# Kernel optimization log

Hardware: AMD Instinct MI355X
Metric: run time of the kernel (lower is better)

The kernel has to match this reference:

```python
import jax, jax.numpy as jnp
import numpy as np

B_, L_, DM, E, H, R, K = 8, 2048, 512, 64, 64, 4, 3

def setup_inputs() -> dict:
    key = jax.random.key(0)
    ks = jax.random.split(key, 9)
    s = 0.02
    x = jax.random.normal(ks[0], (B_, L_, DM), dtype=jnp.float32)
    W_in = jax.random.normal(ks[1], (DM, 2 * E), dtype=jnp.float32) * s
    conv_w = jax.random.normal(ks[2], (E, K), dtype=jnp.float32) * s   # depthwise kernel per channel
    conv_b = jnp.zeros((E,), dtype=jnp.float32)
    W_x = jax.random.normal(ks[3], (E, R + 2 * H), dtype=jnp.float32) * s
    W_dt = jax.random.normal(ks[4], (R, E), dtype=jnp.float32) * s
    b_dt = jax.random.normal(ks[5], (E,), dtype=jnp.float32) * s
    A_log = jnp.log(jnp.broadcast_to(jnp.arange(1, H + 1, dtype=jnp.float32), (E, H)))
    D = jnp.ones((E,), dtype=jnp.float32)
    W_out = jax.random.normal(ks[6], (E, DM), dtype=jnp.float32) * s
    return {"x": x, "W_in": W_in, "conv_w": conv_w, "conv_b": conv_b,
            "W_x": W_x, "W_dt": W_dt, "b_dt": b_dt, "A_log": A_log, "D": D, "W_out": W_out}

def _causal_dwconv(x, w, b):
    # x: [b, l, E]; w: [E, K]; equivalent to Conv1d(groups=E, padding=K-1)[..., :l]
    xp = jnp.pad(x, ((0, 0), (K - 1, 0), (0, 0)))
    y = b
    for j in range(K):
        y = y + xp[:, j:j + x.shape[1], :] * w[:, j]
    return y

def _mamba(x, W_in, conv_w, conv_b, W_x, W_dt, b_dt, A_log, D, W_out):
    l = x.shape[1]
    xz = x @ W_in                                   # [b, l, 2E]
    xp, res = xz[..., :E], xz[..., E:]
    xp = jax.nn.silu(_causal_dwconv(xp, conv_w, conv_b))
    x_dbl = xp @ W_x                                # [b, l, R+2H]
    dlt, Bm, Cm = x_dbl[..., :R], x_dbl[..., R:R + H], x_dbl[..., R + H:]
    delta = jax.nn.softplus(dlt @ W_dt + b_dt)      # [b, l, E]
    A = -jnp.exp(A_log)                             # [E, H]
    deltaA = jnp.exp(jnp.einsum('bld,dn->bldn', delta, A))
    dBu = jnp.einsum('bld,bln,bld->bldn', delta, Bm, xp)
    state0 = jnp.zeros((x.shape[0], E, H), dtype=x.dtype)
    def step(s, inp):
        dA_t, dBu_t, C_t = inp
        s = dA_t * s + dBu_t                        # [b, E, H]
        y_t = jnp.einsum('bdn,bn->bd', s, C_t)
        return s, y_t
    xs = (jnp.swapaxes(deltaA, 0, 1), jnp.swapaxes(dBu, 0, 1), jnp.swapaxes(Cm, 0, 1))
    _, ys = jax.lax.scan(step, state0, xs)          # [l, b, E]
    y = jnp.swapaxes(ys, 0, 1) + xp * D
    y = y * jax.nn.sigmoid(res)
    return y @ W_out

def reference(x, W_in, conv_w, conv_b, W_x, W_dt, b_dt, A_log, D, W_out):
    return _mamba(x, W_in, conv_w, conv_b, W_x, W_dt, b_dt, A_log, D, W_out)
```

## Files before the change

kernel.cpp:

```cpp
#include <hip/hip_runtime.h>
#include <hip/hip_bf16.h>

#define B_ 8
#define L_ 2048
#define DM 512
#define E_ 64
#define H_ 64
#define R_ 4
#define KC 3
#define BL (B_*L_)
#define NX 132
#define LC 128
#define NCH (L_/LC)

typedef __attribute__((ext_vector_type(8))) short bfrag;
typedef __attribute__((ext_vector_type(4))) float facc;
typedef unsigned int u32;

#define LOG2E 1.4426950408889634f

__device__ __forceinline__ unsigned short f2b(float f) {
  __hip_bfloat16 h = __float2bfloat16(f);
  return *reinterpret_cast<unsigned short*>(&h);
}
__device__ __forceinline__ float b2f16(unsigned short u) {
  return __uint_as_float((unsigned)u << 16);
}
__device__ __forceinline__ bfrag ld_frag(const unsigned short* p) {
  bfrag t;
  __builtin_memcpy(&t, p, 16);
  return t;
}

__global__ __launch_bounds__(64) void k_wfuse(
    const float* __restrict__ Wx, const float* __restrict__ Wdt,
    unsigned short* __restrict__ WFT)
{
  const int n = blockIdx.x;
  const int e = threadIdx.x;
  float v;
  if (n < 64) {
    v = 0.f;
    #pragma unroll
    for (int j = 0; j < R_; ++j)
      v = fmaf(Wx[e * NX + j], Wdt[j * 64 + n], v);
  } else if (n < 128) {
    v = Wx[e * NX + R_ + (n - 64)];
  } else {
    v = Wx[e * NX + R_ + 64 + (n - 128)];
  }
  WFT[n * 64 + e] = f2b(v);
}

__global__ __launch_bounds__(256) void k_gemm_in(
    const float* __restrict__ x, const float* __restrict__ Win,
    float* __restrict__ xp_pre, float* __restrict__ resT)
{
  __shared__ unsigned short As[32][72];
  __shared__ unsigned short Bs[128][72];
  const int tid  = threadIdx.x;
  const int m0   = blockIdx.x * 32;
  const int b    = m0 >> 11;
  const int l0   = m0 & 2047;
  const int lane = tid & 63;
  const int wave = tid >> 6;
  const int mt   = wave & 1;
  const int ng   = wave >> 1;
  const int nl   = lane & 15;
  const int g    = lane >> 4;
  const int ar = tid >> 3;
  const int aq = tid & 7;
  const int bn = tid & 127;
  const int kq = tid >> 7;

  facc acc[4];
  #pragma unroll
  for (int j = 0; j < 4; ++j) acc[j] = (facc)(0.f);

  for (int it = 0; it < 8; ++it) {
    const int k0 = it * 64;
    if (it) __syncthreads();
    #pragma unroll
    for (int p = 0; p < 2; ++p) {
      float4 v = *(const float4*)&x[(size_t)(m0 + ar) * DM + k0 + aq * 8 + 4 * p];
      ushort4 u;
      u.x = f2b(v.x); u.y = f2b(v.y); u.z = f2b(v.z); u.w = f2b(v.w);
      *(ushort4*)&As[ar][aq * 8 + 4 * p] = u;
    }
    #pragma unroll
    for (int p = 0; p < 8; ++p) {
      const float* wp = &Win[(size_t)(k0 + kq * 32 + 4 * p) * 128 + bn];
      ushort4 u;
      u.x = f2b(wp[0]);
      u.y = f2b(wp[128]);
      u.z = f2b(wp[256]);
      u.w = f2b(wp[384]);
      *(ushort4*)&Bs[bn][kq * 32 + 4 * p] = u;
    }
    __syncthreads();
    #pragma unroll
    for (int ks = 0; ks < 2; ++ks) {
      bfrag af = ld_frag(&As[mt * 16 + nl][ks * 32 + g * 8]);
      #pragma unroll
      for (int nt2 = 0; nt2 < 4; ++nt2) {
        bfrag bfr = ld_frag(&Bs[(ng * 4 + nt2) * 16 + nl][ks * 32 + g * 8]);
        acc[nt2] = __builtin_amdgcn_mfma_f32_16x16x32_bf16(af, bfr, acc[nt2], 0, 0, 0);
      }
    }
  }
  #pragma unroll
  for (int nt2 = 0; nt2 < 4; ++nt2) {
    facc a = acc[nt2];
    int c = (ng * 4 + nt2) * 16 + nl;
    int mrow = mt * 16 + 4 * g;
    if (c < 64) {
      #pragma unroll
      for (int r = 0; r < 4; ++r)
        xp_pre[(size_t)(m0 + mrow + r) * 64 + c] = a[r];
    } else {
      *(float4*)&resT[(size_t)(b * 64 + (c - 64)) * L_ + l0 + mrow] =
          make_float4(a[0], a[1], a[2], a[3]);
    }
  }
}

__global__ __launch_bounds__(256) void k_fused(
    const float* __restrict__ xp_pre,
    const float* __restrict__ conv_w, const float* __restrict__ conv_b,
    const unsigned short* __restrict__ WFT, const float* __restrict__ bdt,
    float* __restrict__ xpT, float* __restrict__ deltaT,
    u32* __restrict__ BCm)
{
  __shared__ float raw[66][65];
  __shared__ unsigned short rawb[64][72];
  __shared__ unsigned short WFb[192][72];
  const int tid = threadIdx.x;
  const int t0 = blockIdx.x * 64;
  const int b  = t0 >> 11;
  const int l0 = t0 & 2047;
  for (int fidx = tid; fidx < 66 * 16; fidx += 256) {
    int r = fidx >> 4, cg = fidx & 15;
    int l = l0 - 2 + r;
    float4 v = make_float4(0.f, 0.f, 0.f, 0.f);
    if (l >= 0) v = *(const float4*)&xp_pre[((size_t)b * L_ + l) * 64 + cg * 4];
    raw[r][cg * 4 + 0] = v.x;
    raw[r][cg * 4 + 1] = v.y;
    raw[r][cg * 4 + 2] = v.z;
    raw[r][cg * 4 + 3] = v.w;
  }
  for (int i4 = tid; i4 < 192 * 16; i4 += 256) {
    int n = i4 >> 4, jq = i4 & 15;
    *(ushort4*)&WFb[n][jq * 4] = *(const ushort4*)&WFT[n * 64 + jq * 4];
  }
  __syncthreads();
  const int e  = tid & 63;
  const int tl = tid >> 6;
  const float w0 = conv_w[e * KC + 0], w1 = conv_w[e * KC + 1], w2 = conv_w[e * KC + 2];
  const float cb = conv_b[e];
  float cres[16];
  #pragma unroll
  for (int i = 0; i < 16; ++i) {
    int tok = tl * 16 + i;
    float a = cb;
    a = fmaf(raw[tok + 0][e], w0, a);
    a = fmaf(raw[tok + 1][e], w1, a);
    a = fmaf(raw[tok + 2][e], w2, a);
    cres[i] = a / (1.f + __expf(-a));
  }
  #pragma unroll
  for (int i = 0; i < 16; ++i) rawb[tl * 16 + i][e] = f2b(cres[i]);
  #pragma unroll
  for (int i = 0; i < 16; i += 4)
    *(float4*)&xpT[(size_t)(b * 64 + e) * L_ + l0 + tl * 16 + i] =
        make_float4(cres[i], cres[i + 1], cres[i + 2], cres[i + 3]);
  __syncthreads();
  const int wave = tid >> 6;
  const int lane = tid & 63;
  const int nl   = lane & 15;
  const int g    = lane >> 4;
  facc acc[12];
  #pragma unroll
  for (int j = 0; j < 12; ++j) acc[j] = (facc)(0.f);
  #pragma unroll
  for (int ks = 0; ks < 2; ++ks) {
    bfrag af = ld_frag(&rawb[wave * 16 + nl][ks * 32 + g * 8]);
    #pragma unroll
    for (int nt = 0; nt < 12; ++nt) {
      bfrag bfr = ld_frag(&WFb[nt * 16 + nl][ks * 32 + g * 8]);
      acc[nt] = __builtin_amdgcn_mfma_f32_16x16x32_bf16(af, bfr, acc[nt], 0, 0, 0);
    }
  }
  const int mrow = wave * 16 + 4 * g;
  #pragma unroll
  for (int nt = 0; nt < 4; ++nt) {
    facc a = acc[nt];
    int c = nt * 16 + nl;
    float bias = bdt[c];
    float d0 = a[0] + bias, d1 = a[1] + bias, d2 = a[2] + bias, d3 = a[3] + bias;
    float4 dv;
    dv.x = (d0 > 20.f) ? d0 : log1pf(__expf(d0));
    dv.y = (d1 > 20.f) ? d1 : log1pf(__expf(d1));
    dv.z = (d2 > 20.f) ? d2 : log1pf(__expf(d2));
    dv.w = (d3 > 20.f) ? d3 : log1pf(__expf(d3));
    *(float4*)&deltaT[(size_t)(b * 64 + c) * L_ + l0 + mrow] = dv;
  }
  #pragma unroll
  for (int nt = 4; nt < 8; ++nt) {
    facc aB = acc[nt];
    facc aC = acc[nt + 4];
    int col = (nt - 4) * 16 + nl;
    #pragma unroll
    for (int r = 0; r < 4; ++r)
      BCm[(size_t)(t0 + mrow + r) * 64 + col] =
          (u32)f2b(aB[r]) | ((u32)f2b(aC[r]) << 16);
  }
}

__global__ __launch_bounds__(256) void k_scan1(
    const float* __restrict__ deltaT, const float* __restrict__ xpT,
    const u32* __restrict__ BCm, const float* __restrict__ A_log,
    float* __restrict__ Ssum, float* __restrict__ Pp)
{
  __shared__ float dwA[4][256];
  const int tid = threadIdx.x;
  const int wv  = tid >> 6;
  const int h   = tid & 63;
  const int id  = blockIdx.x * 4 + wv;
  const int c   = id & (NCH - 1);
  if (c == NCH - 1) return;
  const int e = (id >> 4) & 63;
  const int b = id >> 10;
  const float A2 = -__expf(A_log[e * 64 + h]) * LOG2E;
  const size_t beL = (size_t)(b * 64 + e) * L_;
  const int l0 = c * LC;
  float* dw = dwA[wv];
  {
    float2 dv = *(const float2*)&deltaT[beL + l0 + 2 * h];
    float2 xv = *(const float2*)&xpT[beL + l0 + 2 * h];
    *(float2*)&dw[2 * h] = dv;
    *(float2*)&dw[128 + 2 * h] = make_float2(dv.x * xv.x, dv.y * xv.y);
  }
  const u32* bc = &BCm[(size_t)(b * L_ + l0) * 64 + h];
  float s = 0.f, sd = 0.f;
  #pragma unroll 2
  for (int k16 = 0; k16 < 8; ++k16) {
    #pragma unroll
    for (int kk = 0; kk < 16; ++kk) {
      const int k = k16 * 16 + kk;
      float dlt = dw[k];
      float w   = dw[128 + k];
      u32 u = bc[(size_t)k * 64];
      float Bh = __uint_as_float(u << 16);
      s = fmaf(__builtin_amdgcn_exp2f(dlt * A2), s, w * Bh);
      sd += dlt;
    }
  }
  const size_t idx = (size_t)id * 64 + h;
  Ssum[idx] = s;
  Pp[idx]   = __builtin_amdgcn_exp2f(A2 * sd);
}

__global__ __launch_bounds__(256) void k_scan3(
    const float* __restrict__ deltaT, const float* __restrict__ xpT,
    const float* __restrict__ resT, const u32* __restrict__ BCm,
    const float* __restrict__ A_log, const float* __restrict__ Dp,
    const float* __restrict__ Ssum, const float* __restrict__ Pp,
    float* __restrict__ ygT)
{
  __shared__ float tileA[4][16][68];
  __shared__ float bufA[4][512];
  const int tid = threadIdx.x;
  const int wv  = tid >> 6;
  const int h   = tid & 63;
  const int id  = blockIdx.x * 4 + wv;
  const int c   = id & (NCH - 1);
  const int e   = (id >> 4) & 63;
  const int b   = id >> 10;
  const float A2 = -__expf(A_log[e * 64 + h]) * LOG2E;
  const float Dv = Dp[e];
  const size_t beL = (size_t)(b * 64 + e) * L_;
  float (*tile)[68] = tileA[wv];
  float* buf = bufA[wv];
  float s = 0.f;
  const size_t sbase = (size_t)(id & ~(NCH - 1)) * 64 + h;
  for (int cc = 0; cc < c; ++cc)
    s = fmaf(Pp[sbase + (size_t)cc * 64], s, Ssum[sbase + (size_t)cc * 64]);
  const int l0 = c * LC;
  {
    float2 dv = *(const float2*)&deltaT[beL + l0 + 2 * h];
    float2 xv = *(const float2*)&xpT[beL + l0 + 2 * h];
    float2 rv = *(const float2*)&resT[beL + l0 + 2 * h];
    *(float2*)&buf[2 * h]       = dv;
    *(float2*)&buf[128 + 2 * h] = make_float2(dv.x * xv.x, dv.y * xv.y);
    *(float2*)&buf[256 + 2 * h] = xv;
    *(float2*)&buf[384 + 2 * h] = rv;
  }
  const u32* bc = &BCm[(size_t)(b * L_ + l0) * 64 + h];
  const int r = h & 15, q = h >> 4;
  #pragma unroll 2
  for (int k16 = 0; k16 < 8; ++k16) {
    #pragma unroll
    for (int kk = 0; kk < 16; ++kk) {
      const int k = k16 * 16 + kk;
      float dlt = buf[k];
      float w   = buf[128 + k];
      u32 u = bc[(size_t)k * 64];
      s = fmaf(__builtin_amdgcn_exp2f(dlt * A2), s, w * __uint_as_float(u << 16));
      tile[kk][h] = s * __uint_as_float(u & 0xffff0000u);
    }
    float part = 0.f;
    const float4* rp = (const float4*)&tile[r][q * 16];
    #pragma unroll
    for (int jq = 0; jq < 4; ++jq) {
      float4 v = rp[jq];
      part += (v.x + v.y) + (v.z + v.w);
    }
    part += __shfl_xor(part, 16, 64);
    part += __shfl_xor(part, 32, 64);
    if (q == 0) {
      const int lk = k16 * 16 + r;
      float y = fmaf(buf[256 + lk], Dv, part);
      y *= __builtin_amdgcn_rcpf(1.f + __builtin_amdgcn_exp2f(-LOG2E * buf[384 + lk]));
      ygT[beL + l0 + lk] = y;
    }
  }
}

__global__ __launch_bounds__(128) void k_gemm_out(
    const float* __restrict__ ygT, const float* __restrict__ Wout,
    float* __restrict__ out)
{
  __shared__ unsigned short As[64][68];
  __shared__ unsigned short Bs[128][68];
  const int tid  = threadIdx.x;
  const int m0   = (blockIdx.x & 255) * 64;
  const int n0   = (blockIdx.x >> 8) * 128;
  const int b    = m0 >> 11;
  const int l0   = m0 & 2047;
  const int lane = tid & 63;
  const int wave = tid >> 6;
  const int nl   = lane & 15;
  const int g    = lane >> 4;
  #pragma unroll
  for (int p = 0; p < 8; ++p) {
    int fidx = tid + 128 * p;
    int e = fidx >> 4, q = fidx & 15;
    float4 v = *(const float4*)&ygT[(size_t)(b * 64 + e) * L_ + l0 + 4 * q];
    As[4 * q + 0][e] = f2b(v.x);
    As[4 * q + 1][e] = f2b(v.y);
    As[4 * q + 2][e] = f2b(v.z);
    As[4 * q + 3][e] = f2b(v.w);
  }
  #pragma unroll
  for (int p = 0; p < 16; ++p) {
    int fidx = tid + 128 * p;
    int r = fidx >> 5, cq = fidx & 31;
    float4 v = *(const float4*)&Wout[(size_t)r * DM + n0 + 4 * cq];
    Bs[4 * cq + 0][r] = f2b(v.x);
    Bs[4 * cq + 1][r] = f2b(v.y);
    Bs[4 * cq + 2][r] = f2b(v.z);
    Bs[4 * cq + 3][r] = f2b(v.w);
  }
  __syncthreads();
  facc acc[2][8];
  #pragma unroll
  for (int i = 0; i < 2; ++i)
    #pragma unroll
    for (int j = 0; j < 8; ++j)
      acc[i][j] = (facc)(0.f);
  #pragma unroll
  for (int ks = 0; ks < 2; ++ks) {
    bfrag af0 = ld_frag(&As[wave * 32 + nl][ks * 32 + g * 8]);
    bfrag af1 = ld_frag(&As[wave * 32 + 16 + nl][ks * 32 + g * 8]);
    #pragma unroll
    for (int nt = 0; nt < 8; ++nt) {
      bfrag bfr = ld_frag(&Bs[nt * 16 + nl][ks * 32 + g * 8]);
      acc[0][nt] = __builtin_amdgcn_mfma_f32_16x16x32_bf16(af0, bfr, acc[0][nt], 0, 0, 0);
      acc[1][nt] = __builtin_amdgcn_mfma_f32_16x16x32_bf16(af1, bfr, acc[1][nt], 0, 0, 0);
    }
  }
  #pragma unroll
  for (int mt = 0; mt < 2; ++mt) {
    int mrow = m0 + wave * 32 + mt * 16 + 4 * g;
    #pragma unroll
    for (int nt = 0; nt < 8; ++nt) {
      facc a = acc[mt][nt];
      int c = n0 + nt * 16 + nl;
      #pragma unroll
      for (int r = 0; r < 4; ++r)
        out[(size_t)(mrow + r) * DM + c] = a[r];
    }
  }
}

extern "C" void kernel_launch(void* const* d_in, const int* in_sizes, int n_in,
                              void* d_out, int out_size, void* d_ws, size_t ws_size,
                              hipStream_t stream) {
  const float* x      = (const float*)d_in[0];
  const float* Win    = (const float*)d_in[1];
  const float* conv_w = (const float*)d_in[2];
  const float* conv_b = (const float*)d_in[3];
  const float* Wx     = (const float*)d_in[4];
  const float* Wdt    = (const float*)d_in[5];
  const float* bdt    = (const float*)d_in[6];
  const float* A_log  = (const float*)d_in[7];
  const float* Dp     = (const float*)d_in[8];
  const float* Wout   = (const float*)d_in[9];
  float* out = (float*)d_out;

  float* ws = (float*)d_ws;
  const size_t SZ = (size_t)BL * 64;
  const size_t CH = (size_t)B_ * E_ * NCH * 64;
  float* xp_pre = ws + 0 * SZ;
  float* resT   = ws + 1 * SZ;
  float* xpT    = ws + 2 * SZ;
  float* deltaT = ws + 3 * SZ;
  u32*   BCm    = (u32*)(ws + 4 * SZ);
  float* ygT    = ws + 5 * SZ;
  float* Ssum   = ws + 6 * SZ;
  float* Pp     = ws + 6 * SZ + 1 * CH;
  unsigned short* WFT = (unsigned short*)(ws + 6 * SZ + 2 * CH);

  hipLaunchKernelGGL(k_wfuse,    dim3(192),               dim3(64),  0, stream, Wx, Wdt, WFT);
  hipLaunchKernelGGL(k_gemm_in,  dim3(BL / 32),           dim3(256), 0, stream,
                     x, Win, xp_pre, resT);
  hipLaunchKernelGGL(k_fused,    dim3(BL / 64),           dim3(256), 0, stream,
                     xp_pre, conv_w, conv_b, WFT, bdt, xpT, deltaT, BCm);
  hipLaunchKernelGGL(k_scan1,    dim3(B_ * E_ * NCH / 4), dim3(256), 0, stream,
                     deltaT, xpT, BCm, A_log, Ssum, Pp);
  hipLaunchKernelGGL(k_scan3,    dim3(B_ * E_ * NCH / 4), dim3(256), 0, stream,
                     deltaT, xpT, resT, BCm, A_log, Dp, Ssum, Pp, ygT);
  hipLaunchKernelGGL(k_gemm_out, dim3(1024),              dim3(128), 0, stream, ygT, Wout, out);
}
```

Before: 171.3 us.

## Pre-convert W_in to bf16 and split fused projection kernel across two blocks

W_in is converted to bf16 once in the weight-prep kernel, so the input GEMM loads half-width weights instead of converting fp32 on every tile load. The fused conv/projection kernel now launches twice as many blocks. Each token group is handled by two blocks: one computes delta and writes xp, the other computes the B/C projections. This raises parallelism and cuts per-block MFMA and register work, at the cost of recomputing the convolution and reloading xp_pre in both blocks. WinTk reuses the ygT workspace region, which is only written later by the scan kernels.

```diff
diff --git a/kernel.cpp b/kernel.cpp
--- a/kernel.cpp
+++ b/kernel.cpp
@@ -34,8 +34,21 @@
 
 __global__ __launch_bounds__(64) void k_wfuse(
     const float* __restrict__ Wx, const float* __restrict__ Wdt,
-    unsigned short* __restrict__ WFT)
-{
+    const float* __restrict__ Win,
+    unsigned short* __restrict__ WFT, unsigned short* __restrict__ WinTk)
+{
+  if (blockIdx.x >= 192) {
+    const int gid = (blockIdx.x - 192) * 64 + threadIdx.x;
+    const float4* src = (const float4*)Win;
+    #pragma unroll
+    for (int i = gid; i < DM * 128 / 4; i += 4096) {
+      float4 v = src[i];
+      ushort4 u;
+      u.x = f2b(v.x); u.y = f2b(v.y); u.z = f2b(v.z); u.w = f2b(v.w);
+      *(ushort4*)&WinTk[i * 4] = u;
+    }
+    return;
+  }
   const int n = blockIdx.x;
   const int e = threadIdx.x;
   float v;
@@ -53,7 +66,7 @@
 }
 
 __global__ __launch_bounds__(256) void k_gemm_in(
-    const float* __restrict__ x, const float* __restrict__ Win,
+    const float* __restrict__ x, const unsigned short* __restrict__ WinTk,
     float* __restrict__ xp_pre, float* __restrict__ resT)
 {
   __shared__ unsigned short As[32][72];
@@ -89,13 +102,11 @@
     }
     #pragma unroll
     for (int p = 0; p < 8; ++p) {
-      const float* wp = &Win[(size_t)(k0 + kq * 32 + 4 * p) * 128 + bn];
-      ushort4 u;
-      u.x = f2b(wp[0]);
-      u.y = f2b(wp[128]);
-      u.z = f2b(wp[256]);
-      u.w = f2b(wp[384]);
-      *(ushort4*)&Bs[bn][kq * 32 + 4 * p] = u;
+      const unsigned short* wp = &WinTk[(size_t)(k0 + kq * 32 + 4 * p) * 128 + bn];
+      u32 lo = (u32)wp[0]   | ((u32)wp[128] << 16);
+      u32 hi = (u32)wp[256] | ((u32)wp[384] << 16);
+      uint2 uu; uu.x = lo; uu.y = hi;
+      *(uint2*)&Bs[bn][kq * 32 + 4 * p] = uu;
     }
     __syncthreads();
     #pragma unroll
@@ -135,7 +146,9 @@
   __shared__ unsigned short rawb[64][72];
   __shared__ unsigned short WFb[192][72];
   const int tid = threadIdx.x;
-  const int t0 = blockIdx.x * 64;
+  const int grp = blockIdx.x >> 1;
+  const int yh  = blockIdx.x & 1;
+  const int t0 = grp * 64;
   const int b  = t0 >> 11;
   const int l0 = t0 & 2047;
   for (int fidx = tid; fidx < 66 * 16; fidx += 256) {
@@ -148,9 +161,13 @@
     raw[r][cg * 4 + 2] = v.z;
     raw[r][cg * 4 + 3] = v.w;
   }
-  for (int i4 = tid; i4 < 192 * 16; i4 += 256) {
-    int n = i4 >> 4, jq = i4 & 15;
-    *(ushort4*)&WFb[n][jq * 4] = *(const ushort4*)&WFT[n * 64 + jq * 4];
+  {
+    const int nbase = yh ? 64 : 0;
+    const int nrows = yh ? 128 : 64;
+    for (int i4 = tid; i4 < nrows * 16; i4 += 256) {
+      int n = nbase + (i4 >> 4), jq = i4 & 15;
+      *(ushort4*)&WFb[n][jq * 4] = *(const ushort4*)&WFT[n * 64 + jq * 4];
+    }
   }
   __syncthreads();
   const int e  = tid & 63;
@@ -169,50 +186,67 @@
   }
   #pragma unroll
   for (int i = 0; i < 16; ++i) rawb[tl * 16 + i][e] = f2b(cres[i]);
-  #pragma unroll
-  for (int i = 0; i < 16; i += 4)
-    *(float4*)&xpT[(size_t)(b * 64 + e) * L_ + l0 + tl * 16 + i] =
-        make_float4(cres[i], cres[i + 1], cres[i + 2], cres[i + 3]);
+  if (yh == 0) {
+    #pragma unroll
+    for (int i = 0; i < 16; i += 4)
+      *(float4*)&xpT[(size_t)(b * 64 + e) * L_ + l0 + tl * 16 + i] =
+          make_float4(cres[i], cres[i + 1], cres[i + 2], cres[i + 3]);
+  }
   __syncthreads();
   const int wave = tid >> 6;
   const int lane = tid & 63;
   const int nl   = lane & 15;
   const int g    = lane >> 4;
-  facc acc[12];
-  #pragma unroll
-  for (int j = 0; j < 12; ++j) acc[j] = (facc)(0.f);
-  #pragma unroll
-  for (int ks = 0; ks < 2; ++ks) {
-    bfrag af = ld_frag(&rawb[wave * 16 + nl][ks * 32 + g * 8]);
-    #pragma unroll
-    for (int nt = 0; nt < 12; ++nt) {
-      bfrag bfr = ld_frag(&WFb[nt * 16 + nl][ks * 32 + g * 8]);
-      acc[nt] = __builtin_amdgcn_mfma_f32_16x16x32_bf16(af, bfr, acc[nt], 0, 0, 0);
-    }
-  }
   const int mrow = wave * 16 + 4 * g;
-  #pragma unroll
-  for (int nt = 0; nt < 4; ++nt) {
-    facc a = acc[nt];
-    int c = nt * 16 + nl;
-    float bias = bdt[c];
-    float d0 = a[0] + bias, d1 = a[1] + bias, d2 = a[2] + bias, d3 = a[3] + bias;
-    float4 dv;
-    dv.x = (d0 > 20.f) ? d0 : log1pf(__expf(d0));
-    dv.y = (d1 > 20.f) ? d1 : log1pf(__expf(d1));
-    dv.z = (d2 > 20.f) ? d2 : log1pf(__expf(d2));
-    dv.w = (d3 > 20.f) ? d3 : log1pf(__expf(d3));
-    *(float4*)&deltaT[(size_t)(b * 64 + c) * L_ + l0 + mrow] = dv;
-  }
-  #pragma unroll
-  for (int nt = 4; nt < 8; ++nt) {
-    facc aB = acc[nt];
-    facc aC = acc[nt + 4];
-    int col = (nt - 4) * 16 + nl;
-    #pragma unroll
-    for (int r = 0; r < 4; ++r)
-      BCm[(size_t)(t0 + mrow + r) * 64 + col] =
-          (u32)f2b(aB[r]) | ((u32)f2b(aC[r]) << 16);
+  if (yh == 0) {
+    facc acc[4];
+    #pragma unroll
+    for (int j = 0; j < 4; ++j) acc[j] = (facc)(0.f);
+    #pragma unroll
+    for (int ks = 0; ks < 2; ++ks) {
+      bfrag af = ld_frag(&rawb[wave * 16 + nl][ks * 32 + g * 8]);
+      #pragma unroll
+      for (int nt = 0; nt < 4; ++nt) {
+        bfrag bfr = ld_frag(&WFb[nt * 16 + nl][ks * 32 + g * 8]);
+        acc[nt] = __builtin_amdgcn_mfma_f32_16x16x32_bf16(af, bfr, acc[nt], 0, 0, 0);
+      }
+    }
+    #pragma unroll
+    for (int nt = 0; nt < 4; ++nt) {
+      facc a = acc[nt];
+      int c = nt * 16 + nl;
+      float bias = bdt[c];
+      float d0 = a[0] + bias, d1 = a[1] + bias, d2 = a[2] + bias, d3 = a[3] + bias;
+      float4 dv;
+      dv.x = (d0 > 20.f) ? d0 : log1pf(__expf(d0));
+      dv.y = (d1 > 20.f) ? d1 : log1pf(__expf(d1));
+      dv.z = (d2 > 20.f) ? d2 : log1pf(__expf(d2));
+      dv.w = (d3 > 20.f) ? d3 : log1pf(__expf(d3));
+      *(float4*)&deltaT[(size_t)(b * 64 + c) * L_ + l0 + mrow] = dv;
+    }
+  } else {
+    facc acc[8];
+    #pragma unroll
+    for (int j = 0; j < 8; ++j) acc[j] = (facc)(0.f);
+    #pragma unroll
+    for (int ks = 0; ks < 2; ++ks) {
+      bfrag af = ld_frag(&rawb[wave * 16 + nl][ks * 32 + g * 8]);
+      #pragma unroll
+      for (int j = 0; j < 8; ++j) {
+        bfrag bfr = ld_frag(&WFb[(4 + j) * 16 + nl][ks * 32 + g * 8]);
+        acc[j] = __builtin_amdgcn_mfma_f32_16x16x32_bf16(af, bfr, acc[j], 0, 0, 0);
+      }
+    }
+    #pragma unroll
+    for (int j = 0; j < 4; ++j) {
+      facc aB = acc[j];
+      facc aC = acc[4 + j];
+      int col = j * 16 + nl;
+      #pragma unroll
+      for (int r = 0; r < 4; ++r)
+        BCm[(size_t)(t0 + mrow + r) * 64 + col] =
+            (u32)f2b(aB[r]) | ((u32)f2b(aC[r]) << 16);
+    }
   }
 }
 
@@ -420,11 +454,13 @@
   float* Ssum   = ws + 6 * SZ;
   float* Pp     = ws + 6 * SZ + 1 * CH;
   unsigned short* WFT = (unsigned short*)(ws + 6 * SZ + 2 * CH);
-
-  hipLaunchKernelGGL(k_wfuse,    dim3(192),               dim3(64),  0, stream, Wx, Wdt, WFT);
+  unsigned short* WinTk = (unsigned short*)(ws + 5 * SZ);
+
+  hipLaunchKernelGGL(k_wfuse,    dim3(256),               dim3(64),  0, stream,
+                     Wx, Wdt, Win, WFT, WinTk);
   hipLaunchKernelGGL(k_gemm_in,  dim3(BL / 32),           dim3(256), 0, stream,
-                     x, Win, xp_pre, resT);
-  hipLaunchKernelGGL(k_fused,    dim3(BL / 64),           dim3(256), 0, stream,
+                     x, WinTk, xp_pre, resT);
+  hipLaunchKernelGGL(k_fused,    dim3(BL / 32),           dim3(256), 0, stream,
                      xp_pre, conv_w, conv_b, WFT, bdt, xpT, deltaT, BCm);
   hipLaunchKernelGGL(k_scan1,    dim3(B_ * E_ * NCH / 4), dim3(256), 0, stream,
                      deltaT, xpT, BCm, A_log, Ssum, Pp);
```

After: 170.4 us. About the same (-0.5%).
